# Kernel tuning notes

Hardware: AMD Instinct MI355X
Metric: run time of the kernel (lower is better)

Reference implementation:

```python
import jax, jax.numpy as jnp
import numpy as np

STAGES = [80, 40, 20]
INPUT = 640
NUM_CLASSES = 80
B = 32
PRE_NMS = 1000      # top-k candidates fed to NMS (fixed-shape surrogate for full sort)
MAX_DET = 100       # max_num_detections
IOU_TH = 0.5
CLASS_OFF = 4096.0  # batched_nms trick: offset boxes per class so classes never overlap


def setup_inputs() -> dict:
    key = jax.random.key(0)
    ks = jax.random.split(key, 6)
    inp = {}
    for i, s in enumerate(STAGES):
        inp[f"cls{i}"] = jax.random.normal(ks[2 * i], (B, NUM_CLASSES, s, s), dtype=jnp.float32)
        # positive ltrb distances, up to ~64 px
        inp[f"box{i}"] = jax.random.uniform(ks[2 * i + 1], (B, 4, s, s), dtype=jnp.float32) * 64.0
    return inp


def _decode_level(cls, box, stage):
    # cls: [B,C,H,W], box: [B,4,H,W]
    step = INPUT // stage
    cls = jax.nn.sigmoid(jnp.transpose(cls, (0, 2, 3, 1)))   # [B,H,W,C]
    conf = jnp.max(cls, axis=-1)                             # [B,H,W]
    cidx = jnp.argmax(cls, axis=-1)                          # [B,H,W]
    box = jnp.transpose(box, (0, 2, 3, 1))                   # [B,H,W,4]
    grid = jnp.arange(stage, dtype=box.dtype) * step
    gx, gy = jnp.meshgrid(grid, grid, indexing='xy')
    block = jnp.stack([gx, gy], axis=-1)                     # [H,W,2]
    xy1 = block - box[..., :2]
    xy2 = block + box[..., 2:4]
    boxes = jnp.concatenate([xy1, xy2], axis=-1).reshape(box.shape[0], -1, 4)
    return boxes, conf.reshape(conf.shape[0], -1), cidx.reshape(cidx.shape[0], -1)


def _iou_matrix(b):
    # b: [N,4] -> [N,N] pairwise IoU
    area = jnp.maximum(b[:, 2] - b[:, 0], 0.) * jnp.maximum(b[:, 3] - b[:, 1], 0.)
    lt = jnp.maximum(b[:, None, :2], b[None, :, :2])
    rb = jnp.minimum(b[:, None, 2:], b[None, :, 2:])
    wh = jnp.maximum(rb - lt, 0.)
    inter = wh[..., 0] * wh[..., 1]
    return inter / (area[:, None] + area[None, :] - inter + 1e-7)


def _nms_image(boxes, scores, classes):
    # class-aware (batched) NMS via per-class coordinate offset
    off = classes.astype(boxes.dtype) * CLASS_OFF
    ob = boxes + off[:, None]
    s_top, idx = jax.lax.top_k(scores, PRE_NMS)
    b_top = ob[idx]                                          # [PRE,4], score-sorted desc
    iou = _iou_matrix(b_top)
    ar = jnp.arange(PRE_NMS)

    def body(i, supp):
        row = (iou[i] > IOU_TH) & (ar > i)
        return jnp.where(supp[i], supp, supp | row)

    supp = jax.lax.fori_loop(0, PRE_NMS, body, jnp.zeros((PRE_NMS,), bool))
    kept_scores = jnp.where(supp, -jnp.inf, s_top)
    sel_s, sel = jax.lax.top_k(kept_scores, MAX_DET)
    final = idx[sel]                                         # indices into original 8400
    valid = jnp.isfinite(sel_s)
    out_b = jnp.where(valid[:, None], boxes[final], 0.)
    out_s = jnp.where(valid, scores[final], 0.)
    out_c = jnp.where(valid, classes[final], -1)
    return out_b, out_s, out_c


def reference(cls0, box0, cls1, box1, cls2, box2):
    parts = [_decode_level(c, b, s) for c, b, s in
             zip([cls0, cls1, cls2], [box0, box1, box2], STAGES)]
    boxes = jnp.concatenate([p[0] for p in parts], axis=1)    # [B,8400,4]
    scores = jnp.concatenate([p[1] for p in parts], axis=1)   # [B,8400]
    classes = jnp.concatenate([p[2] for p in parts], axis=1)  # [B,8400]
    ob, os_, oc = jax.vmap(_nms_image)(boxes, scores, classes)
    boxes_with_scores = jnp.concatenate([ob, os_[..., None]], axis=-1)  # [B,MAX_DET,5]
    return boxes_with_scores, oc
```

## Files before the change

### kernel.cpp

```cpp
#include <hip/hip_runtime.h>

typedef unsigned int u32;
typedef unsigned long long u64;

#define NB 32
#define NCLS 80
#define NANCHOR 8400
#define PRE 1000
#define MAXDET 100
#define NT 1024

__global__ __launch_bounds__(256) void decode_kernel(
        const float* __restrict__ cls0, const float* __restrict__ box0,
        const float* __restrict__ cls1, const float* __restrict__ box1,
        const float* __restrict__ cls2, const float* __restrict__ box2,
        float* __restrict__ ws_scores, float4* __restrict__ ws_boxes,
        int* __restrict__ ws_cls) {
    const int NQ = NANCHOR / 4;
    const int lane = threadIdx.x & 63;
    const int wv = threadIdx.x >> 6;
    const int q = blockIdx.x * 64 + lane;
    int b = q / NQ;
    int r = (q - b * NQ) * 4;

    const float* cp; const float* bp;
    int HW, hw, rowlen, step;
    if (r < 6400) {
        cp = cls0 + (size_t)b * NCLS * 6400; bp = box0 + (size_t)b * 4 * 6400;
        HW = 6400; hw = r;        rowlen = 80; step = 8;
    } else if (r < 8000) {
        cp = cls1 + (size_t)b * NCLS * 1600; bp = box1 + (size_t)b * 4 * 1600;
        HW = 1600; hw = r - 6400; rowlen = 40; step = 16;
    } else {
        cp = cls2 + (size_t)b * NCLS * 400;  bp = box2 + (size_t)b * 4 * 400;
        HW = 400;  hw = r - 8000; rowlen = 20; step = 32;
    }

    __shared__ float s_m[4][4][64];
    __shared__ int   s_c[4][4][64];

    {
        const float* cps = cp + (size_t)(wv * 20) * HW + hw;
        float4 m = *(const float4*)cps;
        int c0 = wv * 20, c1 = c0, c2 = c0, c3 = c0;
#pragma unroll
        for (int c = 1; c < 20; ++c) {
            float4 v = *(const float4*)(cps + (size_t)c * HW);
            int cc = wv * 20 + c;
            if (v.x > m.x) { m.x = v.x; c0 = cc; }
            if (v.y > m.y) { m.y = v.y; c1 = cc; }
            if (v.z > m.z) { m.z = v.z; c2 = cc; }
            if (v.w > m.w) { m.w = v.w; c3 = cc; }
        }
        s_m[wv][0][lane] = m.x; s_c[wv][0][lane] = c0;
        s_m[wv][1][lane] = m.y; s_c[wv][1][lane] = c1;
        s_m[wv][2][lane] = m.z; s_c[wv][2][lane] = c2;
        s_m[wv][3][lane] = m.w; s_c[wv][3][lane] = c3;
    }
    __syncthreads();

    if (wv == 0) {
        float mm[4]; int cc[4];
#pragma unroll
        for (int j = 0; j < 4; ++j) {
            float mv = s_m[0][j][lane]; int cv = s_c[0][j][lane];
#pragma unroll
            for (int s = 1; s < 4; ++s) {
                float v = s_m[s][j][lane];
                if (v > mv) { mv = v; cv = s_c[s][j][lane]; }
            }
            mm[j] = mv; cc[j] = cv;
        }

        float4 L  = *(const float4*)(bp + hw);
        float4 T  = *(const float4*)(bp + HW + hw);
        float4 R  = *(const float4*)(bp + 2 * HW + hw);
        float4 Bo = *(const float4*)(bp + 3 * HW + hw);

        int h = hw / rowlen, w = hw - h * rowlen;
        float gy  = (float)(h * step);
        float gx0 = (float)(w * step);
        float gx1 = gx0 + (float)step;
        float gx2 = gx1 + (float)step;
        float gx3 = gx2 + (float)step;

        int g = b * NANCHOR + r;
        float4 sc;
        sc.x = 1.0f / (1.0f + expf(-mm[0]));
        sc.y = 1.0f / (1.0f + expf(-mm[1]));
        sc.z = 1.0f / (1.0f + expf(-mm[2]));
        sc.w = 1.0f / (1.0f + expf(-mm[3]));
        *(float4*)(ws_scores + g) = sc;
        ws_boxes[g + 0] = make_float4(gx0 - L.x, gy - T.x, gx0 + R.x, gy + Bo.x);
        ws_boxes[g + 1] = make_float4(gx1 - L.y, gy - T.y, gx1 + R.y, gy + Bo.y);
        ws_boxes[g + 2] = make_float4(gx2 - L.z, gy - T.z, gx2 + R.z, gy + Bo.z);
        ws_boxes[g + 3] = make_float4(gx3 - L.w, gy - T.w, gx3 + R.w, gy + Bo.w);
        *(int4*)(ws_cls + g) = make_int4(cc[0], cc[1], cc[2], cc[3]);
    }
}

__device__ __forceinline__ u64 shfl_xor_u64(u64 v, int m) {
    u32 lo = (u32)v, hi = (u32)(v >> 32);
    lo = (u32)__shfl_xor((int)lo, m, 64);
    hi = (u32)__shfl_xor((int)hi, m, 64);
    return ((u64)hi << 32) | (u64)lo;
}

__device__ __forceinline__ u64 readlane_u64(u64 v, int l) {
    u32 lo = (u32)v, hi = (u32)(v >> 32);
    lo = (u32)__builtin_amdgcn_readlane((int)lo, l);
    hi = (u32)__builtin_amdgcn_readlane((int)hi, l);
    return ((u64)hi << 32) | (u64)lo;
}

__device__ __forceinline__ void suffix_scan_1024(int* sh, int* swsum, int* swadd) {
    const int tid = threadIdx.x, lane = tid & 63, wv = tid >> 6;
    int s = sh[tid];
#pragma unroll
    for (int off = 1; off < 64; off <<= 1) {
        int u = __shfl_down(s, off, 64);
        if (lane + off < 64) s += u;
    }
    if (lane == 0) swsum[wv] = s;
    __syncthreads();
    if (tid < 64) {
        int t = (lane < 16) ? swsum[lane] : 0;
#pragma unroll
        for (int off = 1; off < 16; off <<= 1) {
            int u = __shfl_down(t, off, 64);
            if (lane + off < 64) t += u;
        }
        int ab = __shfl_down(t, 1, 64);
        if (lane < 16) swadd[lane] = (lane == 15) ? 0 : ab;
    }
    __syncthreads();
    sh[tid] = s + swadd[wv];
    __syncthreads();
}

__global__ __launch_bounds__(NT) void select_sort_kernel(
        const float* __restrict__ ws_scores, const float4* __restrict__ ws_boxes,
        const int* __restrict__ ws_cls, u64* __restrict__ ws_keys,
        float* __restrict__ ws_sx1, float* __restrict__ ws_sy1,
        float* __restrict__ ws_sx2, float* __restrict__ ws_sy2,
        float* __restrict__ ws_sar) {
    const int b = blockIdx.x;
    const int tid = threadIdx.x;

    __shared__ int s_hist[1024];
    __shared__ u64 s_key[2048];
    __shared__ int s_wsum[16], s_wadd[16];
    __shared__ int s_C, s_base, s_cnt;
    __shared__ u32 s_thresh;

    const float* sc = ws_scores + (size_t)b * NANCHOR;

    s_hist[tid] = 0;
    s_key[tid] = 0ULL;
    s_key[tid + 1024] = 0ULL;
    if (tid == 0) s_cnt = 0;
    __syncthreads();

    u32 sb[9];
#pragma unroll
    for (int k = 0; k < 9; ++k) {
        int a = tid + k * NT;
        if (a < NANCHOR) {
            u32 x = __float_as_uint(sc[a]);
            sb[k] = x;
            atomicAdd(&s_hist[x >> 20], 1);
        } else sb[k] = 0;
    }
    __syncthreads();
    suffix_scan_1024(s_hist, s_wsum, s_wadd);
    {
        int sfx = s_hist[tid];
        int nxt = (tid < 1023) ? s_hist[tid + 1] : 0;
        if (sfx >= PRE && (tid == 1023 || nxt < PRE)) { s_C = tid; s_base = nxt; }
    }
    __syncthreads();
    const int C = s_C, base = s_base;
    s_hist[tid] = 0;
    __syncthreads();

#pragma unroll
    for (int k = 0; k < 9; ++k) {
        int a = tid + k * NT;
        if (a < NANCHOR && (int)(sb[k] >> 20) == C)
            atomicAdd(&s_hist[(sb[k] >> 10) & 1023], 1);
    }
    __syncthreads();
    suffix_scan_1024(s_hist, s_wsum, s_wadd);
    {
        int sfx = base + s_hist[tid];
        int nxt = base + ((tid < 1023) ? s_hist[tid + 1] : 0);
        if (sfx >= PRE && (tid == 1023 || nxt < PRE))
            s_thresh = ((u32)C << 20) | ((u32)tid << 10);
    }
    __syncthreads();
    const u32 thresh = s_thresh;

#pragma unroll
    for (int k = 0; k < 9; ++k) {
        int a = tid + k * NT;
        if (a < NANCHOR && sb[k] >= thresh) {
            int pos = atomicAdd(&s_cnt, 1);
            if (pos < 2048)
                s_key[pos] = ((u64)sb[k] << 14) | (u64)(NANCHOR - 1 - a);
        }
    }
    __syncthreads();
    const int cnt = s_cnt;

    if (cnt > 1024) {
        bool prevBig = false;
        for (int k = 2; k <= 2048; k <<= 1) {
            for (int j = k >> 1; j > 0; j >>= 1) {
                const bool big = (j >= 64);
                if (big || prevBig) __syncthreads();
                else __builtin_amdgcn_wave_barrier();
                for (int i = tid; i < 2048; i += NT) {
                    int ixj = i ^ j;
                    if (ixj > i) {
                        u64 va = s_key[i], vb = s_key[ixj];
                        bool desc = ((i & k) == 0);
                        if (desc ? (va < vb) : (va > vb)) { s_key[i] = vb; s_key[ixj] = va; }
                    }
                }
                prevBig = big;
            }
        }
        __syncthreads();
    } else {
        if (tid >= cnt) s_key[tid] = (u64)tid;
        __syncthreads();
        const u64 my = s_key[tid];
        int rank = 0;
#pragma unroll 4
        for (int j = 0; j < 1024; j += 4) {
            u64 k0 = s_key[j + 0], k1 = s_key[j + 1];
            u64 k2 = s_key[j + 2], k3 = s_key[j + 3];
            rank += (int)(k0 > my) + (int)(k1 > my) + (int)(k2 > my) + (int)(k3 > my);
        }
        __syncthreads();
        s_key[rank] = my;
        __syncthreads();
    }

    {
        u64 key = s_key[tid];
        ws_keys[(b << 10) + tid] = key;
        int idx = (NANCHOR - 1) - (int)(key & 16383ULL);
        float4 bx = ws_boxes[(size_t)b * NANCHOR + idx];
        int c = ws_cls[(size_t)b * NANCHOR + idx];
        float off = (float)c * 4096.0f;
        float x1 = bx.x + off, y1 = bx.y + off, x2 = bx.z + off, y2 = bx.w + off;
        int o = (b << 10) + tid;
        ws_sx1[o] = x1; ws_sy1[o] = y1; ws_sx2[o] = x2; ws_sy2[o] = y2;
        ws_sar[o] = fmaxf(x2 - x1, 0.0f) * fmaxf(y2 - y1, 0.0f);
    }
}

__global__ __launch_bounds__(1024) void iou_bits_kernel(
        const float* __restrict__ ws_sx1, const float* __restrict__ ws_sy1,
        const float* __restrict__ ws_sx2, const float* __restrict__ ws_sy2,
        const float* __restrict__ ws_sar,
        u64* __restrict__ ws_bits, u64* __restrict__ ws_diag) {
    const int blk = blockIdx.x;
    const int b = blk >> 4, tile = blk & 15;
    const int tid = threadIdx.x;

    __shared__ float sx1[1024], sy1[1024], sx2[1024], sy2[1024], sar[1024];
    {
        int o = (b << 10) + tid;
        sx1[tid] = ws_sx1[o]; sy1[tid] = ws_sy1[o];
        sx2[tid] = ws_sx2[o]; sy2[tid] = ws_sy2[o];
        sar[tid] = ws_sar[o];
    }
    __syncthreads();

    const int rl = tid & 63, w = tid >> 6;
    const int r = (tile << 6) + rl;
    u64 bits = 0ULL;
    if (r < 1000 && w >= tile) {
        float xi1 = sx1[r], yi1 = sy1[r], xi2 = sx2[r], yi2 = sy2[r], ai = sar[r];
        const int jbase = w << 6;
#pragma unroll 8
        for (int kb = 0; kb < 64; ++kb) {
            int j = jbase + kb;
            float lx = fmaxf(xi1, sx1[j]);
            float ly = fmaxf(yi1, sy1[j]);
            float rx = fminf(xi2, sx2[j]);
            float ry = fminf(yi2, sy2[j]);
            float wx = fmaxf(rx - lx, 0.0f);
            float wy = fmaxf(ry - ly, 0.0f);
            float inter = wx * wy;
            float iou = inter / (ai + sar[j] - inter + 1e-7f);
            bits |= (iou > 0.5f) ? (1ULL << kb) : 0ULL;
        }
        u64 mlow;
        if (w == tile) {
            int bpos = r & 63;
            mlow = (bpos == 63) ? 0ULL : (~0ULL << (bpos + 1));
        } else mlow = ~0ULL;
        u64 mhigh = (jbase + 64 <= 1000) ? ~0ULL : ((1ULL << (1000 - jbase)) - 1ULL);
        bits &= mlow & mhigh;
    }
    ws_bits[((size_t)b << 14) + ((size_t)r << 4) + w] = bits;
    if (w == tile) ws_diag[(b << 10) + r] = bits;
}

__global__ __launch_bounds__(128) void nms_scan_kernel(
        const u64* __restrict__ ws_bits, const u64* __restrict__ ws_diag,
        const u64* __restrict__ ws_keys, const float4* __restrict__ ws_boxes,
        const int* __restrict__ ws_cls, float* __restrict__ out) {
    const int b = blockIdx.x;
    const int tid = threadIdx.x;

    __shared__ int s_keep[MAXDET];
    __shared__ int s_nk;

    if (tid < 64) {
        const int lane = tid;
        const u64* bits = ws_bits + ((size_t)b << 14);
        const u64* diag = ws_diag + ((size_t)b << 10);
        int nkept = 0;
        for (int wi = 0; wi < 16 && nkept < MAXDET; ++wi) {
            const int wbase = wi << 6;
            u64 acc = 0ULL;
            if (lane < nkept)       acc  = bits[((size_t)s_keep[lane] << 4) + wi];
            if (lane + 64 < nkept)  acc |= bits[((size_t)s_keep[lane + 64] << 4) + wi];
#pragma unroll
            for (int off = 32; off > 0; off >>= 1) acc |= shfl_xor_u64(acc, off);
            u64 cur = acc;
            u64 rw = diag[wbase + lane];
            const int nb = (wbase + 64 <= 1000) ? 64 : (1000 - wbase);
            for (int bit = 0; bit < nb; ++bit) {
                if (!((cur >> bit) & 1ULL)) {
                    if (lane == 0) s_keep[nkept] = wbase + bit;
                    nkept++;
                    if (nkept >= MAXDET) break;
                    cur |= readlane_u64(rw, bit);
                }
            }
        }
        if (lane == 0) s_nk = nkept;
    }
    __syncthreads();

    const int nk = s_nk;
    if (tid < MAXDET) {
        float* o = out + ((size_t)b * MAXDET + tid) * 5;
        float* oc = out + (size_t)NB * MAXDET * 5 + (size_t)b * MAXDET + tid;
        if (tid < nk) {
            int rank = s_keep[tid];
            u64 key = ws_keys[(b << 10) + rank];
            int idx = (NANCHOR - 1) - (int)(key & 16383ULL);
            float score = __uint_as_float((u32)(key >> 14));
            float4 bx = ws_boxes[(size_t)b * NANCHOR + idx];
            int c = ws_cls[(size_t)b * NANCHOR + idx];
            o[0] = bx.x; o[1] = bx.y; o[2] = bx.z; o[3] = bx.w; o[4] = score;
            *oc = (float)c;
        } else {
            o[0] = 0.0f; o[1] = 0.0f; o[2] = 0.0f; o[3] = 0.0f; o[4] = 0.0f;
            *oc = -1.0f;
        }
    }
}

extern "C" void kernel_launch(void* const* d_in, const int* in_sizes, int n_in,
                              void* d_out, int out_size, void* d_ws, size_t ws_size,
                              hipStream_t stream) {
    const float* cls0 = (const float*)d_in[0];
    const float* box0 = (const float*)d_in[1];
    const float* cls1 = (const float*)d_in[2];
    const float* box1 = (const float*)d_in[3];
    const float* cls2 = (const float*)d_in[4];
    const float* box2 = (const float*)d_in[5];

    float* ws = (float*)d_ws;
    float* ws_scores = ws;
    float4* ws_boxes = (float4*)(ws + NB * NANCHOR);
    int* ws_cls = (int*)(ws + (size_t)NB * NANCHOR * 5);
    float* base6 = ws + (size_t)NB * NANCHOR * 6;
    u64* ws_keys = (u64*)base6;
    float* ws_sx1 = base6 + 65536;
    float* ws_sy1 = ws_sx1 + NB * 1024;
    float* ws_sx2 = ws_sy1 + NB * 1024;
    float* ws_sy2 = ws_sx2 + NB * 1024;
    float* ws_sar = ws_sy2 + NB * 1024;
    u64* ws_bits = (u64*)(ws_sar + NB * 1024);
    u64* ws_diag = ws_bits + (size_t)NB * 1024 * 16;

    int nquads = NB * (NANCHOR / 4);
    decode_kernel<<<nquads / 64, 256, 0, stream>>>(
        cls0, box0, cls1, box1, cls2, box2, ws_scores, ws_boxes, ws_cls);

    select_sort_kernel<<<NB, NT, 0, stream>>>(ws_scores, ws_boxes, ws_cls, ws_keys,
                                              ws_sx1, ws_sy1, ws_sx2, ws_sy2, ws_sar);

    iou_bits_kernel<<<NB * 16, 1024, 0, stream>>>(ws_sx1, ws_sy1, ws_sx2, ws_sy2, ws_sar,
                                                  ws_bits, ws_diag);

    nms_scan_kernel<<<NB, 128, 0, stream>>>(ws_bits, ws_diag, ws_keys, ws_boxes, ws_cls,
                                            (float*)d_out);
}
```

Measured before the change: 184.3 us.

## Spread decode epilogue over all threads and gather sorted boxes inside IoU kernel

The decode kernel's second phase now uses all 256 threads, each finishing one anchor, instead of only wave 0 handling four anchors. This spreads the sigmoid, box decode and stores across the whole block. The per-candidate gather of boxes, class offset and area moves from the single-block-per-image sort kernel into the IoU kernel, which reads keys and gathers directly into shared memory. That drops the intermediate SoA workspace arrays and shortens the serial tail of the sort kernel, at the cost of the gather being repeated by each of the 16 tiles per image.

Measured after the change: 186.6 us. No clear change (+1.2%).

```diff
diff --git a/kernel.cpp b/kernel.cpp
--- a/kernel.cpp
+++ b/kernel.cpp
@@ -19,27 +19,25 @@
     const int NQ = NANCHOR / 4;
     const int lane = threadIdx.x & 63;
     const int wv = threadIdx.x >> 6;
-    const int q = blockIdx.x * 64 + lane;
-    int b = q / NQ;
-    int r = (q - b * NQ) * 4;
-
-    const float* cp; const float* bp;
-    int HW, hw, rowlen, step;
-    if (r < 6400) {
-        cp = cls0 + (size_t)b * NCLS * 6400; bp = box0 + (size_t)b * 4 * 6400;
-        HW = 6400; hw = r;        rowlen = 80; step = 8;
-    } else if (r < 8000) {
-        cp = cls1 + (size_t)b * NCLS * 1600; bp = box1 + (size_t)b * 4 * 1600;
-        HW = 1600; hw = r - 6400; rowlen = 40; step = 16;
-    } else {
-        cp = cls2 + (size_t)b * NCLS * 400;  bp = box2 + (size_t)b * 4 * 400;
-        HW = 400;  hw = r - 8000; rowlen = 20; step = 32;
-    }
-
-    __shared__ float s_m[4][4][64];
-    __shared__ int   s_c[4][4][64];
-
-    {
+
+    __shared__ float s_m[4][256];
+    __shared__ int   s_c[4][256];
+
+    {
+        const int q = blockIdx.x * 64 + lane;
+        int b = q / NQ;
+        int r = (q - b * NQ) * 4;
+
+        const float* cp;
+        int HW, hw;
+        if (r < 6400) {
+            cp = cls0 + (size_t)b * NCLS * 6400; HW = 6400; hw = r;
+        } else if (r < 8000) {
+            cp = cls1 + (size_t)b * NCLS * 1600; HW = 1600; hw = r - 6400;
+        } else {
+            cp = cls2 + (size_t)b * NCLS * 400;  HW = 400;  hw = r - 8000;
+        }
+
         const float* cps = cp + (size_t)(wv * 20) * HW + hw;
         float4 m = *(const float4*)cps;
         int c0 = wv * 20, c1 = c0, c2 = c0, c3 = c0;
@@ -52,50 +50,52 @@
             if (v.z > m.z) { m.z = v.z; c2 = cc; }
             if (v.w > m.w) { m.w = v.w; c3 = cc; }
         }
-        s_m[wv][0][lane] = m.x; s_c[wv][0][lane] = c0;
-        s_m[wv][1][lane] = m.y; s_c[wv][1][lane] = c1;
-        s_m[wv][2][lane] = m.z; s_c[wv][2][lane] = c2;
-        s_m[wv][3][lane] = m.w; s_c[wv][3][lane] = c3;
-    }
-    __syncthreads();
-
-    if (wv == 0) {
-        float mm[4]; int cc[4];
-#pragma unroll
-        for (int j = 0; j < 4; ++j) {
-            float mv = s_m[0][j][lane]; int cv = s_c[0][j][lane];
-#pragma unroll
-            for (int s = 1; s < 4; ++s) {
-                float v = s_m[s][j][lane];
-                if (v > mv) { mv = v; cv = s_c[s][j][lane]; }
-            }
-            mm[j] = mv; cc[j] = cv;
-        }
-
-        float4 L  = *(const float4*)(bp + hw);
-        float4 T  = *(const float4*)(bp + HW + hw);
-        float4 R  = *(const float4*)(bp + 2 * HW + hw);
-        float4 Bo = *(const float4*)(bp + 3 * HW + hw);
+        int a = lane * 4;
+        s_m[wv][a + 0] = m.x; s_c[wv][a + 0] = c0;
+        s_m[wv][a + 1] = m.y; s_c[wv][a + 1] = c1;
+        s_m[wv][a + 2] = m.z; s_c[wv][a + 2] = c2;
+        s_m[wv][a + 3] = m.w; s_c[wv][a + 3] = c3;
+    }
+    __syncthreads();
+
+    {
+        const int t = threadIdx.x;
+        const int ga = blockIdx.x * 256 + t;
+        int b = ga / NANCHOR;
+        int r = ga - b * NANCHOR;
+
+        const float* bp;
+        int HW, hw, rowlen, step;
+        if (r < 6400) {
+            bp = box0 + (size_t)b * 4 * 6400;
+            HW = 6400; hw = r;        rowlen = 80; step = 8;
+        } else if (r < 8000) {
+            bp = box1 + (size_t)b * 4 * 1600;
+            HW = 1600; hw = r - 6400; rowlen = 40; step = 16;
+        } else {
+            bp = box2 + (size_t)b * 4 * 400;
+            HW = 400;  hw = r - 8000; rowlen = 20; step = 32;
+        }
+
+        float mv = s_m[0][t]; int cv = s_c[0][t];
+#pragma unroll
+        for (int s = 1; s < 4; ++s) {
+            float v = s_m[s][t];
+            if (v > mv) { mv = v; cv = s_c[s][t]; }
+        }
+
+        float l  = bp[hw];
+        float tt = bp[HW + hw];
+        float rr = bp[2 * HW + hw];
+        float bo = bp[3 * HW + hw];
 
         int h = hw / rowlen, w = hw - h * rowlen;
-        float gy  = (float)(h * step);
-        float gx0 = (float)(w * step);
-        float gx1 = gx0 + (float)step;
-        float gx2 = gx1 + (float)step;
-        float gx3 = gx2 + (float)step;
-
-        int g = b * NANCHOR + r;
-        float4 sc;
-        sc.x = 1.0f / (1.0f + expf(-mm[0]));
-        sc.y = 1.0f / (1.0f + expf(-mm[1]));
-        sc.z = 1.0f / (1.0f + expf(-mm[2]));
-        sc.w = 1.0f / (1.0f + expf(-mm[3]));
-        *(float4*)(ws_scores + g) = sc;
-        ws_boxes[g + 0] = make_float4(gx0 - L.x, gy - T.x, gx0 + R.x, gy + Bo.x);
-        ws_boxes[g + 1] = make_float4(gx1 - L.y, gy - T.y, gx1 + R.y, gy + Bo.y);
-        ws_boxes[g + 2] = make_float4(gx2 - L.z, gy - T.z, gx2 + R.z, gy + Bo.z);
-        ws_boxes[g + 3] = make_float4(gx3 - L.w, gy - T.w, gx3 + R.w, gy + Bo.w);
-        *(int4*)(ws_cls + g) = make_int4(cc[0], cc[1], cc[2], cc[3]);
+        float gy = (float)(h * step);
+        float gx = (float)(w * step);
+
+        ws_scores[ga] = 1.0f / (1.0f + expf(-mv));
+        ws_boxes[ga] = make_float4(gx - l, gy - tt, gx + rr, gy + bo);
+        ws_cls[ga] = cv;
     }
 }
 
@@ -139,11 +139,7 @@
 }
 
 __global__ __launch_bounds__(NT) void select_sort_kernel(
-        const float* __restrict__ ws_scores, const float4* __restrict__ ws_boxes,
-        const int* __restrict__ ws_cls, u64* __restrict__ ws_keys,
-        float* __restrict__ ws_sx1, float* __restrict__ ws_sy1,
-        float* __restrict__ ws_sx2, float* __restrict__ ws_sy2,
-        float* __restrict__ ws_sar) {
+        const float* __restrict__ ws_scores, u64* __restrict__ ws_keys) {
     const int b = blockIdx.x;
     const int tid = threadIdx.x;
 
@@ -247,35 +243,27 @@
         __syncthreads();
     }
 
-    {
-        u64 key = s_key[tid];
-        ws_keys[(b << 10) + tid] = key;
+    ws_keys[(b << 10) + tid] = s_key[tid];
+}
+
+__global__ __launch_bounds__(1024) void iou_bits_kernel(
+        const u64* __restrict__ ws_keys, const float4* __restrict__ ws_boxes,
+        const int* __restrict__ ws_cls,
+        u64* __restrict__ ws_bits, u64* __restrict__ ws_diag) {
+    const int blk = blockIdx.x;
+    const int b = blk >> 4, tile = blk & 15;
+    const int tid = threadIdx.x;
+
+    __shared__ float sx1[1024], sy1[1024], sx2[1024], sy2[1024], sar[1024];
+    {
+        u64 key = ws_keys[(b << 10) + tid];
         int idx = (NANCHOR - 1) - (int)(key & 16383ULL);
         float4 bx = ws_boxes[(size_t)b * NANCHOR + idx];
         int c = ws_cls[(size_t)b * NANCHOR + idx];
         float off = (float)c * 4096.0f;
         float x1 = bx.x + off, y1 = bx.y + off, x2 = bx.z + off, y2 = bx.w + off;
-        int o = (b << 10) + tid;
-        ws_sx1[o] = x1; ws_sy1[o] = y1; ws_sx2[o] = x2; ws_sy2[o] = y2;
-        ws_sar[o] = fmaxf(x2 - x1, 0.0f) * fmaxf(y2 - y1, 0.0f);
-    }
-}
-
-__global__ __launch_bounds__(1024) void iou_bits_kernel(
-        const float* __restrict__ ws_sx1, const float* __restrict__ ws_sy1,
-        const float* __restrict__ ws_sx2, const float* __restrict__ ws_sy2,
-        const float* __restrict__ ws_sar,
-        u64* __restrict__ ws_bits, u64* __restrict__ ws_diag) {
-    const int blk = blockIdx.x;
-    const int b = blk >> 4, tile = blk & 15;
-    const int tid = threadIdx.x;
-
-    __shared__ float sx1[1024], sy1[1024], sx2[1024], sy2[1024], sar[1024];
-    {
-        int o = (b << 10) + tid;
-        sx1[tid] = ws_sx1[o]; sy1[tid] = ws_sy1[o];
-        sx2[tid] = ws_sx2[o]; sy2[tid] = ws_sy2[o];
-        sar[tid] = ws_sar[o];
+        sx1[tid] = x1; sy1[tid] = y1; sx2[tid] = x2; sy2[tid] = y2;
+        sar[tid] = fmaxf(x2 - x1, 0.0f) * fmaxf(y2 - y1, 0.0f);
     }
     __syncthreads();
 
@@ -382,24 +370,17 @@
     float* ws_scores = ws;
     float4* ws_boxes = (float4*)(ws + NB * NANCHOR);
     int* ws_cls = (int*)(ws + (size_t)NB * NANCHOR * 5);
-    float* base6 = ws + (size_t)NB * NANCHOR * 6;
-    u64* ws_keys = (u64*)base6;
-    float* ws_sx1 = base6 + 65536;
-    float* ws_sy1 = ws_sx1 + NB * 1024;
-    float* ws_sx2 = ws_sy1 + NB * 1024;
-    float* ws_sy2 = ws_sx2 + NB * 1024;
-    float* ws_sar = ws_sy2 + NB * 1024;
-    u64* ws_bits = (u64*)(ws_sar + NB * 1024);
+    u64* ws_keys = (u64*)(ws + (size_t)NB * NANCHOR * 6);
+    u64* ws_bits = ws_keys + (size_t)NB * 1024;
     u64* ws_diag = ws_bits + (size_t)NB * 1024 * 16;
 
     int nquads = NB * (NANCHOR / 4);
     decode_kernel<<<nquads / 64, 256, 0, stream>>>(
         cls0, box0, cls1, box1, cls2, box2, ws_scores, ws_boxes, ws_cls);
 
-    select_sort_kernel<<<NB, NT, 0, stream>>>(ws_scores, ws_boxes, ws_cls, ws_keys,
-                                              ws_sx1, ws_sy1, ws_sx2, ws_sy2, ws_sar);
-
-    iou_bits_kernel<<<NB * 16, 1024, 0, stream>>>(ws_sx1, ws_sy1, ws_sx2, ws_sy2, ws_sar,
+    select_sort_kernel<<<NB, NT, 0, stream>>>(ws_scores, ws_keys);
+
+    iou_bits_kernel<<<NB * 16, 1024, 0, stream>>>(ws_keys, ws_boxes, ws_cls,
                                                   ws_bits, ws_diag);
 
     nms_scan_kernel<<<NB, 128, 0, stream>>>(ws_bits, ws_diag, ws_keys, ws_boxes, ws_cls,
```
